# Kernel tuning notes

Measured on AMD Instinct MI355X. Metric: run time of the kernel, lower is better.

The kernel has to match this reference:

```python
import jax, jax.numpy as jnp
import numpy as np

B, N, DIM = 8, 8192, 256
HEADS, LOCAL_HEADS, WINDOW = 8, 1, 64
HD = DIM // HEADS  # 32
MLP_HIDDEN = 1024
EPS = 1e-5


def layer_norm(x, g, b):
    mu = jnp.mean(x, axis=-1, keepdims=True)
    var = jnp.var(x, axis=-1, keepdims=True)
    return (x - mu) * jax.lax.rsqrt(var + EPS) * g + b


def look_around(t, pad_value=0.0):
    # t: (b, nw, w, ...); concat windows [i-1, i, i+1] -> (b, nw, 3w, ...)
    nw = t.shape[1]
    pads = [(0, 0), (1, 1)] + [(0, 0)] * (t.ndim - 2)
    p = jnp.pad(t, pads, constant_values=pad_value)
    return jnp.concatenate([p[:, i:i + nw] for i in range(3)], axis=2)


def local_attn(q, k, v):
    # lucidrains LocalAttention, causal=False, look_backward=look_forward=1
    # q,k,v: (b_merged, n, d)
    b, n, d = q.shape
    nw = n // WINDOW
    scale = d ** -0.5
    bq = q.reshape(b, nw, WINDOW, d) * scale
    bk = look_around(k.reshape(b, nw, WINDOW, d))  # (b, nw, 3w, d)
    bv = look_around(v.reshape(b, nw, WINDOW, d))
    ticker = jnp.arange(n).reshape(1, nw, WINDOW)
    bq_k = look_around(ticker, pad_value=-1)       # (1, nw, 3w)
    pad_mask = (bq_k == -1)[:, :, None, :]         # (1, nw, 1, 3w)
    dots = jnp.einsum('bnie,bnje->bnij', bq, bk)   # (b, nw, w, 3w)
    dots = jnp.where(pad_mask, -1e9, dots)
    attn = jax.nn.softmax(dots, axis=-1)
    out = jnp.einsum('bnij,bnje->bnie', attn, bv)
    return out.reshape(b, n, d)


def linear_attn(q, k, v):
    # q,k,v: (b, h, n, d)
    d = q.shape[-1]
    qs = jax.nn.softmax(q, axis=-1) * d ** -0.5
    ks = jax.nn.softmax(k, axis=-2)
    ctx = jnp.einsum('bhnd,bhne->bhde', ks, v)     # (b, h, d, d) tiny
    return jnp.einsum('bhnd,bhde->bhne', qs, ctx)


def setup_inputs() -> dict:
    key = jax.random.key(0)
    ks = jax.random.split(key, 8)
    s = 0.02
    return {
        'x': jax.random.normal(ks[0], (B, N, DIM), jnp.float32),
        'norm1_g': jnp.ones((DIM,), jnp.float32),
        'norm1_b': jnp.zeros((DIM,), jnp.float32),
        'Wq': jax.random.normal(ks[1], (DIM, DIM), jnp.float32) * s,
        'Wkv': jax.random.normal(ks[2], (DIM, DIM), jnp.float32) * s,
        'Wproj': jax.random.normal(ks[3], (DIM, DIM), jnp.float32) * s,
        'bproj': jnp.zeros((DIM,), jnp.float32),
        'norm2_g': jnp.ones((DIM,), jnp.float32),
        'norm2_b': jnp.zeros((DIM,), jnp.float32),
        'W1': jax.random.normal(ks[4], (MLP_HIDDEN, DIM), jnp.float32) * s,
        'b1': jnp.zeros((MLP_HIDDEN,), jnp.float32),
        'W2': jax.random.normal(ks[5], (DIM, MLP_HIDDEN), jnp.float32) * s,
        'b2': jnp.zeros((DIM,), jnp.float32),
    }


def reference(x, norm1_g, norm1_b, Wq, Wkv, Wproj, bproj, norm2_g, norm2_b, W1, b1, W2, b2):
    b, n, c = x.shape
    h = layer_norm(x, norm1_g, norm1_b)
    q = h @ Wq.T
    kv = h @ Wkv.T  # k and v share the same projection in the original code
    split_heads = lambda t: t.reshape(b, n, HEADS, HD).transpose(0, 2, 1, 3)
    q, k, v = split_heads(q), split_heads(kv), split_heads(kv)
    lq, gq = q[:, :LOCAL_HEADS], q[:, LOCAL_HEADS:]
    lk, gk = k[:, :LOCAL_HEADS], k[:, LOCAL_HEADS:]
    lv, gv = v[:, :LOCAL_HEADS], v[:, LOCAL_HEADS:]
    lout = local_attn(lq.reshape(b * LOCAL_HEADS, n, HD),
                      lk.reshape(b * LOCAL_HEADS, n, HD),
                      lv.reshape(b * LOCAL_HEADS, n, HD)).reshape(b, LOCAL_HEADS, n, HD)
    gout = linear_attn(gq, gk, gv)
    attn = jnp.concatenate([lout, gout], axis=1)   # (b, H, n, hd)
    y = attn.transpose(0, 2, 1, 3).reshape(b, n, c) @ Wproj.T + bproj
    x = x + y
    h2 = layer_norm(x, norm2_g, norm2_b)
    m = jax.nn.gelu(h2 @ W1.T + b1, approximate=False) @ W2.T + b2
    return x + m
```

## Files before the change

kernel.cpp:

```cpp
#include <hip/hip_runtime.h>
#include <hip/hip_bf16.h>

typedef __bf16 bf16;
typedef __bf16 bf16x8 __attribute__((ext_vector_type(8)));
typedef float f32x4 __attribute__((ext_vector_type(4)));

__device__ __forceinline__ void gld16(const void* g, void* l) {
  __builtin_amdgcn_global_load_lds((const __attribute__((address_space(1))) void*)g,
                                   (__attribute__((address_space(3))) void*)l, 16, 0, 0);
}

__global__ void cvt_weights(const float* __restrict__ wq, const float* __restrict__ wkv,
                            const float* __restrict__ wp, const float* __restrict__ w1,
                            const float* __restrict__ w2,
                            bf16* __restrict__ wqkv, bf16* __restrict__ wpb,
                            bf16* __restrict__ w1b, bf16* __restrict__ w2b) {
  int i = blockIdx.x * 256 + threadIdx.x;
  if (i < 65536) wqkv[i] = (bf16)wq[i];
  else if (i < 131072) wqkv[i] = (bf16)wkv[i - 65536];
  else if (i < 196608) wpb[i - 131072] = (bf16)wp[i - 131072];
  else if (i < 458752) w1b[i - 196608] = (bf16)w1[i - 196608];
  else if (i < 720896) w2b[i - 458752] = (bf16)w2[i - 458752];
}

__launch_bounds__(256)
__global__ void ln_kernel(const float* __restrict__ x, const float* __restrict__ g,
                          const float* __restrict__ b, bf16* __restrict__ out) {
  const int row = blockIdx.x * 4 + (threadIdx.x >> 6);
  const int lane = threadIdx.x & 63;
  const float4 v = ((const float4*)(x + (long)row * 256))[lane];
  float s = v.x + v.y + v.z + v.w;
#pragma unroll
  for (int o = 1; o < 64; o <<= 1) s += __shfl_xor(s, o);
  const float mu = s * (1.f / 256.f);
  const float dx = v.x - mu, dy = v.y - mu, dz = v.z - mu, dw = v.w - mu;
  float q = dx * dx + dy * dy + dz * dz + dw * dw;
#pragma unroll
  for (int o = 1; o < 64; o <<= 1) q += __shfl_xor(q, o);
  const float rstd = rsqrtf(q * (1.f / 256.f) + 1e-5f);
  const float4 gg = ((const float4*)g)[lane];
  const float4 bb = ((const float4*)b)[lane];
  union { bf16 h[4]; uint2 u; } pk;
  pk.h[0] = (bf16)(dx * rstd * gg.x + bb.x);
  pk.h[1] = (bf16)(dy * rstd * gg.y + bb.y);
  pk.h[2] = (bf16)(dz * rstd * gg.z + bb.z);
  pk.h[3] = (bf16)(dw * rstd * gg.w + bb.w);
  *(uint2*)(out + (long)row * 256 + lane * 4) = pk.u;
}

template <int EPI>
__launch_bounds__(256)
__global__ void gemm_kernel(const bf16* __restrict__ A, const bf16* __restrict__ B,
                            void* C, const float* __restrict__ bias,
                            const float* res, int Nn, int K) {
  __shared__ bf16 Alds[128 * 64];
  __shared__ bf16 Blds[128 * 64];
  const int tid = threadIdx.x;
  const int w = tid >> 6, lane = tid & 63;
  const int wr = w >> 1, wc = w & 1;
  const long m0 = (long)blockIdx.y * 128;
  const long n0 = (long)blockIdx.x * 128;
  const int srow = lane >> 3;
  const int scol = (lane & 7) * 8;
  f32x4 acc[4][4] = {};
  for (int kt = 0; kt < K; kt += 64) {
#pragma unroll
    for (int i = 0; i < 4; ++i) {
      const int c = w * 4 + i;
      const int row = c * 8 + srow;
      gld16(A + (m0 + row) * K + kt + scol, Alds + c * 512);
      gld16(B + (n0 + row) * K + kt + scol, Blds + c * 512);
    }
    asm volatile("s_waitcnt vmcnt(0)" ::: "memory");
    __syncthreads();
#pragma unroll
    for (int ks = 0; ks < 2; ++ks) {
      const int colo = ks * 32 + (lane >> 4) * 8;
      bf16x8 af[4], bfr[4];
#pragma unroll
      for (int fm = 0; fm < 4; ++fm)
        af[fm] = *(const bf16x8*)(Alds + (wr * 64 + fm * 16 + (lane & 15)) * 64 + colo);
#pragma unroll
      for (int fn = 0; fn < 4; ++fn)
        bfr[fn] = *(const bf16x8*)(Blds + (wc * 64 + fn * 16 + (lane & 15)) * 64 + colo);
#pragma unroll
      for (int fm = 0; fm < 4; ++fm)
#pragma unroll
        for (int fn = 0; fn < 4; ++fn)
          acc[fm][fn] = __builtin_amdgcn_mfma_f32_16x16x32_bf16(af[fm], bfr[fn], acc[fm][fn], 0, 0, 0);
    }
    __syncthreads();
  }
#pragma unroll
  for (int fm = 0; fm < 4; ++fm)
#pragma unroll
    for (int fn = 0; fn < 4; ++fn)
#pragma unroll
      for (int r = 0; r < 4; ++r) {
        const long row = m0 + wr * 64 + fm * 16 + (lane >> 4) * 4 + r;
        const long col = n0 + wc * 64 + fn * 16 + (lane & 15);
        const long idx = row * Nn + col;
        const float v = acc[fm][fn][r];
        if constexpr (EPI == 0) {
          ((bf16*)C)[idx] = (bf16)v;
        } else if constexpr (EPI == 1) {
          ((float*)C)[idx] = v + bias[col] + res[idx];
        } else {
          const float t = v + bias[col];
          ((bf16*)C)[idx] = (bf16)(0.5f * t * (1.f + erff(t * 0.70710678118654752f)));
        }
      }
}

__launch_bounds__(256)
__global__ void lattn_kernel(const bf16* __restrict__ qkv, bf16* __restrict__ attn) {
  const int j = blockIdx.x, b = blockIdx.y;
  const int tid = threadIdx.x, w = tid >> 6, lane = tid & 63;
  __shared__ bf16 Qs[64 * 40];
  __shared__ bf16 Ks[192 * 40];
  __shared__ bf16 Kt[32 * 200];
  __shared__ bf16 Ps[4][16 * 200];
  const float scale = 0.17677669529663687f;
  const long base = (long)b * 8192 + (long)j * 64;
  for (int i = tid; i < 64 * 32; i += 256) {
    const int r = i >> 5, d = i & 31;
    Qs[r * 40 + d] = (bf16)((float)qkv[(base + r) * 512 + d] * scale);
  }
  for (int i = tid; i < 192 * 32; i += 256) {
    const int c = i >> 5, d = i & 31;
    const long tc = (long)j * 64 - 64 + c;
    float kv = 0.f;
    if (tc >= 0 && tc < 8192) kv = (float)qkv[((long)b * 8192 + tc) * 512 + 256 + d];
    const bf16 kb = (bf16)kv;
    Ks[c * 40 + d] = kb;
    Kt[d * 200 + c] = kb;
  }
  __syncthreads();
  const int l15 = lane & 15, l4 = lane >> 4;
  const bf16x8 aq = *(const bf16x8*)(Qs + (w * 16 + l15) * 40 + l4 * 8);
  const f32x4 zz = {0.f, 0.f, 0.f, 0.f};
  f32x4 S[12];
#pragma unroll
  for (int fn = 0; fn < 12; ++fn) {
    const bf16x8 bk = *(const bf16x8*)(Ks + (fn * 16 + l15) * 40 + l4 * 8);
    S[fn] = __builtin_amdgcn_mfma_f32_16x16x32_bf16(aq, bk, zz, 0, 0, 0);
  }
#pragma unroll
  for (int fn = 0; fn < 12; ++fn) {
    const long tc = (long)j * 64 - 64 + fn * 16 + l15;
    if (tc < 0 || tc >= 8192) { S[fn][0] = -1e9f; S[fn][1] = -1e9f; S[fn][2] = -1e9f; S[fn][3] = -1e9f; }
  }
  float sinv[4];
#pragma unroll
  for (int r = 0; r < 4; ++r) {
    float m = -1e30f;
#pragma unroll
    for (int fn = 0; fn < 12; ++fn) m = fmaxf(m, S[fn][r]);
#pragma unroll
    for (int o = 1; o < 16; o <<= 1) m = fmaxf(m, __shfl_xor(m, o));
    float s = 0.f;
#pragma unroll
    for (int fn = 0; fn < 12; ++fn) { const float e = __expf(S[fn][r] - m); S[fn][r] = e; s += e; }
#pragma unroll
    for (int o = 1; o < 16; o <<= 1) s += __shfl_xor(s, o);
    sinv[r] = 1.f / s;
  }
#pragma unroll
  for (int fn = 0; fn < 12; ++fn)
#pragma unroll
    for (int r = 0; r < 4; ++r)
      Ps[w][(l4 * 4 + r) * 200 + fn * 16 + l15] = (bf16)(S[fn][r] * sinv[r]);
  __syncthreads();
  f32x4 O[2] = {};
#pragma unroll
  for (int ks = 0; ks < 6; ++ks) {
    const bf16x8 ap = *(const bf16x8*)(Ps[w] + l15 * 200 + ks * 32 + l4 * 8);
#pragma unroll
    for (int fe = 0; fe < 2; ++fe) {
      const bf16x8 bv = *(const bf16x8*)(Kt + (fe * 16 + l15) * 200 + ks * 32 + l4 * 8);
      O[fe] = __builtin_amdgcn_mfma_f32_16x16x32_bf16(ap, bv, O[fe], 0, 0, 0);
    }
  }
#pragma unroll
  for (int fe = 0; fe < 2; ++fe)
#pragma unroll
    for (int r = 0; r < 4; ++r)
      attn[(base + w * 16 + l4 * 4 + r) * 256 + fe * 16 + l15] = (bf16)O[fe][r];
}

__launch_bounds__(256)
__global__ void ctx_kernel(const bf16* __restrict__ qkv, float* __restrict__ ctx,
                           float* __restrict__ S) {
  const int bh = blockIdx.x;
  const int b = bh / 7, h = bh % 7 + 1;
  const int tid = threadIdx.x;
  const int w = tid >> 6, lane = tid & 63;
  const int l15 = lane & 15, l4 = lane >> 4;
  __shared__ bf16 evT[32 * 264];
  __shared__ bf16 kT[48 * 264];
  __shared__ float red[4][32 * 48];
  const long n0 = (long)blockIdx.y * 256;
  const bf16* kp = qkv + ((long)b * 8192 + n0 + tid) * 512 + 256 + h * 32;
  bf16x8 kv[4];
#pragma unroll
  for (int c = 0; c < 4; ++c) kv[c] = *(const bf16x8*)(kp + c * 8);
#pragma unroll
  for (int i = 0; i < 16; ++i)
    kT[(32 + i) * 264 + tid] = (i == 0) ? (bf16)1.0f : (bf16)0.0f;
#pragma unroll
  for (int c = 0; c < 4; ++c)
#pragma unroll
    for (int j = 0; j < 8; ++j) {
      const int d = c * 8 + j;
      evT[d * 264 + tid] = (bf16)__expf((float)kv[c][j]);
      kT[d * 264 + tid] = kv[c][j];
    }
  __syncthreads();
  f32x4 acc[2][3] = {};
#pragma unroll
  for (int ks = 0; ks < 2; ++ks) {
    const int ncol = w * 64 + ks * 32 + l4 * 8;
    bf16x8 af[2], bb[3];
#pragma unroll
    for (int fm = 0; fm < 2; ++fm) af[fm] = *(const bf16x8*)(evT + (fm * 16 + l15) * 264 + ncol);
#pragma unroll
    for (int fe = 0; fe < 3; ++fe) bb[fe] = *(const bf16x8*)(kT + (fe * 16 + l15) * 264 + ncol);
#pragma unroll
    for (int fm = 0; fm < 2; ++fm)
#pragma unroll
      for (int fe = 0; fe < 3; ++fe)
        acc[fm][fe] = __builtin_amdgcn_mfma_f32_16x16x32_bf16(af[fm], bb[fe], acc[fm][fe], 0, 0, 0);
  }
#pragma unroll
  for (int fm = 0; fm < 2; ++fm)
#pragma unroll
    for (int fe = 0; fe < 3; ++fe)
#pragma unroll
      for (int r = 0; r < 4; ++r)
        red[w][(fm * 16 + l4 * 4 + r) * 48 + fe * 16 + l15] = acc[fm][fe][r];
  __syncthreads();
  for (int i = tid; i < 32 * 48; i += 256) {
    const float v = red[0][i] + red[1][i] + red[2][i] + red[3][i];
    const int d = i / 48, e = i - d * 48;
    if (e < 32) atomicAdd(ctx + (long)bh * 1024 + d * 32 + e, v);
    else if (e == 32) atomicAdd(S + bh * 32 + d, v);
  }
}

__launch_bounds__(256)
__global__ void lout_kernel(const bf16* __restrict__ qkv, const float* __restrict__ S,
                            const float* __restrict__ ctx, bf16* __restrict__ attn) {
  const int bh = blockIdx.x;
  const int b = bh / 7, h = bh % 7 + 1;
  const int tid = threadIdx.x;
  const int w = tid >> 6, lane = tid & 63;
  const int l15 = lane & 15, l4 = lane >> 4;
  __shared__ bf16 qs[256 * 40];
  __shared__ bf16 C2t[32 * 40];
  const long n0 = (long)blockIdx.y * 256;
  for (int i = tid; i < 1024; i += 256) {
    const int e = i >> 5, d = i & 31;
    C2t[e * 40 + d] = (bf16)(ctx[(long)bh * 1024 + d * 32 + e] / S[bh * 32 + d]);
  }
  const bf16* qp = qkv + ((long)b * 8192 + n0 + tid) * 512 + h * 32;
  bf16x8 qv[4];
#pragma unroll
  for (int c = 0; c < 4; ++c) qv[c] = *(const bf16x8*)(qp + c * 8);
  float qf[32];
#pragma unroll
  for (int c = 0; c < 4; ++c)
#pragma unroll
    for (int j = 0; j < 8; ++j) qf[c * 8 + j] = (float)qv[c][j];
  float m = qf[0];
#pragma unroll
  for (int d = 1; d < 32; ++d) m = fmaxf(m, qf[d]);
  float s = 0.f;
#pragma unroll
  for (int d = 0; d < 32; ++d) { qf[d] = __expf(qf[d] - m); s += qf[d]; }
  const float f = 0.17677669529663687f / s;
#pragma unroll
  for (int c = 0; c < 4; ++c) {
    bf16x8 o;
#pragma unroll
    for (int j = 0; j < 8; ++j) o[j] = (bf16)(qf[c * 8 + j] * f);
    *(bf16x8*)(qs + tid * 40 + c * 8) = o;
  }
  __syncthreads();
  f32x4 acc[4][2] = {};
  bf16x8 bfr[2];
#pragma unroll
  for (int fe = 0; fe < 2; ++fe) bfr[fe] = *(const bf16x8*)(C2t + (fe * 16 + l15) * 40 + l4 * 8);
#pragma unroll
  for (int fm = 0; fm < 4; ++fm) {
    const bf16x8 af = *(const bf16x8*)(qs + (w * 64 + fm * 16 + l15) * 40 + l4 * 8);
#pragma unroll
    for (int fe = 0; fe < 2; ++fe)
      acc[fm][fe] = __builtin_amdgcn_mfma_f32_16x16x32_bf16(af, bfr[fe], acc[fm][fe], 0, 0, 0);
  }
#pragma unroll
  for (int fm = 0; fm < 4; ++fm)
#pragma unroll
    for (int fe = 0; fe < 2; ++fe)
#pragma unroll
      for (int r = 0; r < 4; ++r)
        attn[((long)b * 8192 + n0 + w * 64 + fm * 16 + l4 * 4 + r) * 256 + h * 32 + fe * 16 + l15]
            = (bf16)acc[fm][fe][r];
}

extern "C" void kernel_launch(void* const* d_in, const int* in_sizes, int n_in,
                              void* d_out, int out_size, void* d_ws, size_t ws_size,
                              hipStream_t stream) {
  const float* x     = (const float*)d_in[0];
  const float* n1g   = (const float*)d_in[1];
  const float* n1b   = (const float*)d_in[2];
  const float* Wq    = (const float*)d_in[3];
  const float* Wkv   = (const float*)d_in[4];
  const float* Wproj = (const float*)d_in[5];
  const float* bproj = (const float*)d_in[6];
  const float* n2g   = (const float*)d_in[7];
  const float* n2b   = (const float*)d_in[8];
  const float* W1    = (const float*)d_in[9];
  const float* b1    = (const float*)d_in[10];
  const float* W2    = (const float*)d_in[11];
  const float* b2    = (const float*)d_in[12];
  float* out = (float*)d_out;
  char* ws = (char*)d_ws;

  bf16* wqkv   = (bf16*)(ws + 0);
  bf16* wprojb = (bf16*)(ws + 262144);
  bf16* w1b    = (bf16*)(ws + 393216);
  bf16* w2b    = (bf16*)(ws + 917504);
  float* Sbuf  = (float*)(ws + 1441792);
  float* ctx   = (float*)(ws + 1448960);
  bf16* hbuf   = (bf16*)(ws + 1685504);
  bf16* qkv    = (bf16*)(ws + 35239936);
  bf16* hidden = qkv;

  cvt_weights<<<2816, 256, 0, stream>>>(Wq, Wkv, Wproj, W1, W2, wqkv, wprojb, w1b, w2b);
  ln_kernel<<<16384, 256, 0, stream>>>(x, n1g, n1b, hbuf);
  gemm_kernel<0><<<dim3(4, 512), 256, 0, stream>>>(hbuf, wqkv, qkv, nullptr, nullptr, 512, 256);
  hipMemsetAsync(Sbuf, 0, 7168 + 229376, stream);
  lattn_kernel<<<dim3(128, 8), 256, 0, stream>>>(qkv, hbuf);
  ctx_kernel<<<dim3(56, 32), 256, 0, stream>>>(qkv, ctx, Sbuf);
  lout_kernel<<<dim3(56, 32), 256, 0, stream>>>(qkv, Sbuf, ctx, hbuf);
  gemm_kernel<1><<<dim3(2, 512), 256, 0, stream>>>(hbuf, wprojb, out, bproj, x, 256, 256);
  ln_kernel<<<16384, 256, 0, stream>>>(out, n2g, n2b, hbuf);
  gemm_kernel<2><<<dim3(8, 512), 256, 0, stream>>>(hbuf, w1b, hidden, b1, nullptr, 1024, 256);
  gemm_kernel<1><<<dim3(2, 512), 256, 0, stream>>>(hidden, w2b, out, b2, out, 256, 1024);
}
```

Before: 412.2 us.

## Restructure GEMMs: stream A through swizzled double-buffered LDS, read B directly from global

Replaces the 128x128 LDS-tiled GEMM with a 512-thread kernel whose block covers 64 rows and the full N tile (up to 512 columns). Only A goes through LDS, as XOR-swizzled, double-buffered K chunks loaded asynchronously. B fragments are loaded straight from global memory and rely on cache reuse across blocks. The aim is to avoid re-reading A per column tile, cut LDS traffic and bank conflicts, and overlap loads with MFMA work, at the cost of more register pressure and uncached-path global loads for B.

```diff
diff --git a/kernel.cpp b/kernel.cpp
--- a/kernel.cpp
+++ b/kernel.cpp
@@ -48,58 +48,79 @@
   *(uint2*)(out + (long)row * 256 + lane * 4) = pk.u;
 }
 
-template <int EPI>
-__launch_bounds__(256)
-__global__ void gemm_kernel(const bf16* __restrict__ A, const bf16* __restrict__ B,
-                            void* C, const float* __restrict__ bias,
-                            const float* res, int Nn, int K) {
-  __shared__ bf16 Alds[128 * 64];
-  __shared__ bf16 Blds[128 * 64];
+template <int EPI, int MT, int NTILE, int KK, int NCHUNK>
+__launch_bounds__(512, 4)
+__global__ void gemm_bd(const bf16* __restrict__ A, const bf16* __restrict__ B,
+                        void* C, const float* __restrict__ bias,
+                        const float* res, int ldC) {
+  constexpr int CW = NTILE / 8;
+  constexpr int FM = MT / 16;
+  constexpr int FN = CW / 16;
+  constexpr int CK = KK / NCHUNK;
+  constexpr int RSB = 2 * CK;
+  constexpr int LROW = (RSB == 256) ? 8 : ((RSB == 512) ? 9 : 10);
+  constexpr int CHB = MT * CK * 2;
+  constexpr int ITER = CHB / (512 * 16);
+  __shared__ bf16 lds[2 * MT * CK];
   const int tid = threadIdx.x;
   const int w = tid >> 6, lane = tid & 63;
-  const int wr = w >> 1, wc = w & 1;
-  const long m0 = (long)blockIdx.y * 128;
-  const long n0 = (long)blockIdx.x * 128;
-  const int srow = lane >> 3;
-  const int scol = (lane & 7) * 8;
-  f32x4 acc[4][4] = {};
-  for (int kt = 0; kt < K; kt += 64) {
-#pragma unroll
-    for (int i = 0; i < 4; ++i) {
-      const int c = w * 4 + i;
-      const int row = c * 8 + srow;
-      gld16(A + (m0 + row) * K + kt + scol, Alds + c * 512);
-      gld16(B + (n0 + row) * K + kt + scol, Blds + c * 512);
-    }
-    asm volatile("s_waitcnt vmcnt(0)" ::: "memory");
-    __syncthreads();
-#pragma unroll
-    for (int ks = 0; ks < 2; ++ks) {
-      const int colo = ks * 32 + (lane >> 4) * 8;
-      bf16x8 af[4], bfr[4];
-#pragma unroll
-      for (int fm = 0; fm < 4; ++fm)
-        af[fm] = *(const bf16x8*)(Alds + (wr * 64 + fm * 16 + (lane & 15)) * 64 + colo);
-#pragma unroll
-      for (int fn = 0; fn < 4; ++fn)
-        bfr[fn] = *(const bf16x8*)(Blds + (wc * 64 + fn * 16 + (lane & 15)) * 64 + colo);
-#pragma unroll
-      for (int fm = 0; fm < 4; ++fm)
-#pragma unroll
-        for (int fn = 0; fn < 4; ++fn)
-          acc[fm][fn] = __builtin_amdgcn_mfma_f32_16x16x32_bf16(af[fm], bfr[fn], acc[fm][fn], 0, 0, 0);
-    }
-    __syncthreads();
-  }
-#pragma unroll
-  for (int fm = 0; fm < 4; ++fm)
-#pragma unroll
-    for (int fn = 0; fn < 4; ++fn)
+  const int l15 = lane & 15, l4 = lane >> 4;
+  const int swz = (l15 & 7) << 4;
+  const long m0 = (long)blockIdx.x * MT;
+  const int n_base = blockIdx.y * NTILE;
+  const bf16* Bl = B + ((long)(n_base + w * CW + l15)) * KK + l4 * 8;
+
+  f32x4 acc[FM][FN] = {};
+
+  auto stage = [&](int c, int buf) {
+#pragma unroll
+    for (int it = 0; it < ITER; ++it) {
+      const int p = it * 8192 + tid * 16;
+      const int row = p >> LROW;
+      const int colb = (p & (RSB - 1)) ^ ((row & 7) << 4);
+      gld16((const char*)A + ((m0 + row) * KK + (long)c * CK) * 2 + colb,
+            (char*)lds + buf * CHB + it * 8192 + w * 1024);
+    }
+  };
+
+  stage(0, 0);
+  asm volatile("s_waitcnt vmcnt(0)" ::: "memory");
+  __syncthreads();
+
+  for (int c = 0; c < NCHUNK; ++c) {
+    if (c + 1 < NCHUNK) stage(c + 1, (c + 1) & 1);
+    const char* base = (const char*)lds + (c & 1) * CHB;
+#pragma unroll
+    for (int kl = 0; kl < CK / 32; ++kl) {
+      bf16x8 bfrag[FN];
+#pragma unroll
+      for (int fn = 0; fn < FN; ++fn)
+        bfrag[fn] = *(const bf16x8*)(Bl + (long)fn * 16 * KK + c * CK + kl * 32);
+      bf16x8 afrag[FM];
+#pragma unroll
+      for (int fm = 0; fm < FM; ++fm)
+        afrag[fm] = *(const bf16x8*)(base + (fm * 16 + l15) * RSB + ((kl * 64 + l4 * 16) ^ swz));
+#pragma unroll
+      for (int fm = 0; fm < FM; ++fm)
+#pragma unroll
+        for (int fn = 0; fn < FN; ++fn)
+          acc[fm][fn] = __builtin_amdgcn_mfma_f32_16x16x32_bf16(afrag[fm], bfrag[fn], acc[fm][fn], 0, 0, 0);
+    }
+    if (c + 1 < NCHUNK) {
+      asm volatile("s_waitcnt vmcnt(0)" ::: "memory");
+      __syncthreads();
+    }
+  }
+
+#pragma unroll
+  for (int fm = 0; fm < FM; ++fm)
+#pragma unroll
+    for (int fn = 0; fn < FN; ++fn)
 #pragma unroll
       for (int r = 0; r < 4; ++r) {
-        const long row = m0 + wr * 64 + fm * 16 + (lane >> 4) * 4 + r;
-        const long col = n0 + wc * 64 + fn * 16 + (lane & 15);
-        const long idx = row * Nn + col;
+        const long row = m0 + fm * 16 + l4 * 4 + r;
+        const int col = n_base + w * CW + fn * 16 + l15;
+        const long idx = row * ldC + col;
         const float v = acc[fm][fn][r];
         if constexpr (EPI == 0) {
           ((bf16*)C)[idx] = (bf16)v;
@@ -338,13 +359,13 @@
 
   cvt_weights<<<2816, 256, 0, stream>>>(Wq, Wkv, Wproj, W1, W2, wqkv, wprojb, w1b, w2b);
   ln_kernel<<<16384, 256, 0, stream>>>(x, n1g, n1b, hbuf);
-  gemm_kernel<0><<<dim3(4, 512), 256, 0, stream>>>(hbuf, wqkv, qkv, nullptr, nullptr, 512, 256);
+  gemm_bd<0, 64, 512, 256, 2><<<dim3(1024, 1), 512, 0, stream>>>(hbuf, wqkv, qkv, nullptr, nullptr, 512);
   hipMemsetAsync(Sbuf, 0, 7168 + 229376, stream);
   lattn_kernel<<<dim3(128, 8), 256, 0, stream>>>(qkv, hbuf);
   ctx_kernel<<<dim3(56, 32), 256, 0, stream>>>(qkv, ctx, Sbuf);
   lout_kernel<<<dim3(56, 32), 256, 0, stream>>>(qkv, Sbuf, ctx, hbuf);
-  gemm_kernel<1><<<dim3(2, 512), 256, 0, stream>>>(hbuf, wprojb, out, bproj, x, 256, 256);
+  gemm_bd<1, 64, 256, 256, 2><<<dim3(1024, 1), 512, 0, stream>>>(hbuf, wprojb, out, bproj, x, 256);
   ln_kernel<<<16384, 256, 0, stream>>>(out, n2g, n2b, hbuf);
-  gemm_kernel<2><<<dim3(8, 512), 256, 0, stream>>>(hbuf, w1b, hidden, b1, nullptr, 1024, 256);
-  gemm_kernel<1><<<dim3(2, 512), 256, 0, stream>>>(hidden, w2b, out, b2, out, 256, 1024);
-}
+  gemm_bd<2, 64, 512, 256, 2><<<dim3(1024, 2), 512, 0, stream>>>(hbuf, w1b, hidden, b1, nullptr, 1024);
+  gemm_bd<1, 64, 256, 1024, 4><<<dim3(1024, 1), 512, 0, stream>>>(hidden, w2b, out, b2, out, 256);
+}
```

New measurement: 403.2 us. -2.2%, faster.

## Replace LDS-tiled GEMM with register-resident weight GEMMs and XCD-aware block mapping

Applied to the files above, without the earlier changes.

Replaces the shared-memory tiled 128x128 GEMM with kernels where each wave holds a 64-column slice of the weight matrix in registers for the full K=256 and streams 64 rows of A directly from global memory into registers. LDS staging and the barriers around it go away, and a block-index remap spreads consecutive slots across the 8 XCDs. The K=1024 MLP down-projection gets its own kernel that reloads weight chunks per K-chunk and accumulates into the output in place. The trade-offs are heavy register pressure (the 2-blocks-per-SM launch bound may force spills), redundant global reads of weights by every wave, and uncoalesced 16-byte-per-lane A loads that no longer share tiles across waves.

```diff
diff --git a/kernel.cpp b/kernel.cpp
--- a/kernel.cpp
+++ b/kernel.cpp
@@ -4,11 +4,6 @@
 typedef __bf16 bf16;
 typedef __bf16 bf16x8 __attribute__((ext_vector_type(8)));
 typedef float f32x4 __attribute__((ext_vector_type(4)));
-
-__device__ __forceinline__ void gld16(const void* g, void* l) {
-  __builtin_amdgcn_global_load_lds((const __attribute__((address_space(1))) void*)g,
-                                   (__attribute__((address_space(3))) void*)l, 16, 0, 0);
-}
 
 __global__ void cvt_weights(const float* __restrict__ wq, const float* __restrict__ wkv,
                             const float* __restrict__ wp, const float* __restrict__ w1,
@@ -48,68 +43,129 @@
   *(uint2*)(out + (long)row * 256 + lane * 4) = pk.u;
 }
 
-template <int EPI>
-__launch_bounds__(256)
-__global__ void gemm_kernel(const bf16* __restrict__ A, const bf16* __restrict__ B,
-                            void* C, const float* __restrict__ bias,
-                            const float* res, int Nn, int K) {
-  __shared__ bf16 Alds[128 * 64];
-  __shared__ bf16 Blds[128 * 64];
-  const int tid = threadIdx.x;
-  const int w = tid >> 6, lane = tid & 63;
-  const int wr = w >> 1, wc = w & 1;
-  const long m0 = (long)blockIdx.y * 128;
-  const long n0 = (long)blockIdx.x * 128;
-  const int srow = lane >> 3;
-  const int scol = (lane & 7) * 8;
-  f32x4 acc[4][4] = {};
-  for (int kt = 0; kt < K; kt += 64) {
-#pragma unroll
-    for (int i = 0; i < 4; ++i) {
-      const int c = w * 4 + i;
-      const int row = c * 8 + srow;
-      gld16(A + (m0 + row) * K + kt + scol, Alds + c * 512);
-      gld16(B + (n0 + row) * K + kt + scol, Blds + c * 512);
+template <int EPI, int NCG, int NBLK>
+__launch_bounds__(256, 2)
+__global__ void gemm_reg(const bf16* __restrict__ A, const bf16* __restrict__ Bw,
+                         void* C, const float* __restrict__ bias,
+                         const float* __restrict__ res, int ldC) {
+  const int tid = threadIdx.x, w = tid >> 6, lane = tid & 63;
+  const int l15 = lane & 15, l4 = lane >> 4;
+  const int bid = blockIdx.x;
+  const int slot4 = ((bid & 7) * (NBLK / 8) + (bid >> 3)) * 4 + w;
+  const int cg = slot4 % NCG;
+  const long row0 = (long)(slot4 / NCG) * 64;
+  const int c0 = cg * 64;
+
+  bf16x8 Breg[8][4];
+  {
+    const bf16* Bp = Bw + ((long)c0 + l15) * 256 + l4 * 8;
+#pragma unroll
+    for (int kl = 0; kl < 8; ++kl)
+#pragma unroll
+      for (int fn = 0; fn < 4; ++fn)
+        Breg[kl][fn] = *(const bf16x8*)(Bp + fn * (16 * 256) + kl * 32);
+  }
+  float biasr[4];
+  if constexpr (EPI != 0) {
+#pragma unroll
+    for (int fn = 0; fn < 4; ++fn) biasr[fn] = bias[c0 + fn * 16 + l15];
+  }
+
+#pragma unroll
+  for (int mi = 0; mi < 2; ++mi) {
+    const long r0 = row0 + mi * 32;
+    bf16x8 Areg[2][8];
+    const bf16* Ap = A + (r0 + l15) * 256 + l4 * 8;
+#pragma unroll
+    for (int fm = 0; fm < 2; ++fm)
+#pragma unroll
+      for (int kl = 0; kl < 8; ++kl)
+        Areg[fm][kl] = *(const bf16x8*)(Ap + fm * (16 * 256) + kl * 32);
+    f32x4 acc[2][4] = {};
+#pragma unroll
+    for (int kl = 0; kl < 8; ++kl)
+#pragma unroll
+      for (int fm = 0; fm < 2; ++fm)
+#pragma unroll
+        for (int fn = 0; fn < 4; ++fn)
+          acc[fm][fn] = __builtin_amdgcn_mfma_f32_16x16x32_bf16(Areg[fm][kl], Breg[kl][fn],
+                                                                acc[fm][fn], 0, 0, 0);
+#pragma unroll
+    for (int fm = 0; fm < 2; ++fm)
+#pragma unroll
+      for (int fn = 0; fn < 4; ++fn)
+#pragma unroll
+        for (int r = 0; r < 4; ++r) {
+          const long row = r0 + fm * 16 + l4 * 4 + r;
+          const long col = c0 + fn * 16 + l15;
+          const long idx = row * ldC + col;
+          const float v = acc[fm][fn][r];
+          if constexpr (EPI == 0) {
+            ((bf16*)C)[idx] = (bf16)v;
+          } else if constexpr (EPI == 1) {
+            ((float*)C)[idx] = v + biasr[fn] + res[idx];
+          } else {
+            const float t = v + biasr[fn];
+            ((bf16*)C)[idx] = (bf16)(0.5f * t * (1.f + erff(t * 0.70710678118654752f)));
+          }
+        }
+  }
+}
+
+__launch_bounds__(256, 2)
+__global__ void gemm_mlp2(const bf16* __restrict__ A, const bf16* __restrict__ Bw,
+                          float* __restrict__ C, const float* __restrict__ bias) {
+  constexpr int NBLK = 1024, NCG = 4;
+  const int tid = threadIdx.x, w = tid >> 6, lane = tid & 63;
+  const int l15 = lane & 15, l4 = lane >> 4;
+  const int bid = blockIdx.x;
+  const int slot4 = ((bid & 7) * (NBLK / 8) + (bid >> 3)) * 4 + w;
+  const int cg = slot4 % NCG;
+  const long row0 = (long)(slot4 / NCG) * 64;
+  const int c0 = cg * 64;
+  float biasr[4];
+#pragma unroll
+  for (int fn = 0; fn < 4; ++fn) biasr[fn] = bias[c0 + fn * 16 + l15];
+
+#pragma unroll
+  for (int mi = 0; mi < 2; ++mi) {
+    const long r0 = row0 + mi * 32;
+    f32x4 acc[2][4] = {};
+    for (int kc = 0; kc < 4; ++kc) {
+      bf16x8 Breg[8][4];
+      const bf16* Bp = Bw + ((long)c0 + l15) * 1024 + kc * 256 + l4 * 8;
+#pragma unroll
+      for (int kl = 0; kl < 8; ++kl)
+#pragma unroll
+        for (int fn = 0; fn < 4; ++fn)
+          Breg[kl][fn] = *(const bf16x8*)(Bp + fn * (16 * 1024) + kl * 32);
+      bf16x8 Areg[2][8];
+      const bf16* Ap = A + (r0 + l15) * 1024 + kc * 256 + l4 * 8;
+#pragma unroll
+      for (int fm = 0; fm < 2; ++fm)
+#pragma unroll
+        for (int kl = 0; kl < 8; ++kl)
+          Areg[fm][kl] = *(const bf16x8*)(Ap + fm * (16 * 1024) + kl * 32);
+#pragma unroll
+      for (int kl = 0; kl < 8; ++kl)
+#pragma unroll
+        for (int fm = 0; fm < 2; ++fm)
+#pragma unroll
+          for (int fn = 0; fn < 4; ++fn)
+            acc[fm][fn] = __builtin_amdgcn_mfma_f32_16x16x32_bf16(Areg[fm][kl], Breg[kl][fn],
+                                                                  acc[fm][fn], 0, 0, 0);
     }
-    asm volatile("s_waitcnt vmcnt(0)" ::: "memory");
-    __syncthreads();
-#pragma unroll
-    for (int ks = 0; ks < 2; ++ks) {
-      const int colo = ks * 32 + (lane >> 4) * 8;
-      bf16x8 af[4], bfr[4];
-#pragma unroll
-      for (int fm = 0; fm < 4; ++fm)
-        af[fm] = *(const bf16x8*)(Alds + (wr * 64 + fm * 16 + (lane & 15)) * 64 + colo);
+#pragma unroll
+    for (int fm = 0; fm < 2; ++fm)
 #pragma unroll
       for (int fn = 0; fn < 4; ++fn)
-        bfr[fn] = *(const bf16x8*)(Blds + (wc * 64 + fn * 16 + (lane & 15)) * 64 + colo);
-#pragma unroll
-      for (int fm = 0; fm < 4; ++fm)
-#pragma unroll
-        for (int fn = 0; fn < 4; ++fn)
-          acc[fm][fn] = __builtin_amdgcn_mfma_f32_16x16x32_bf16(af[fm], bfr[fn], acc[fm][fn], 0, 0, 0);
-    }
-    __syncthreads();
-  }
-#pragma unroll
-  for (int fm = 0; fm < 4; ++fm)
-#pragma unroll
-    for (int fn = 0; fn < 4; ++fn)
-#pragma unroll
-      for (int r = 0; r < 4; ++r) {
-        const long row = m0 + wr * 64 + fm * 16 + (lane >> 4) * 4 + r;
-        const long col = n0 + wc * 64 + fn * 16 + (lane & 15);
-        const long idx = row * Nn + col;
-        const float v = acc[fm][fn][r];
-        if constexpr (EPI == 0) {
-          ((bf16*)C)[idx] = (bf16)v;
-        } else if constexpr (EPI == 1) {
-          ((float*)C)[idx] = v + bias[col] + res[idx];
-        } else {
-          const float t = v + bias[col];
-          ((bf16*)C)[idx] = (bf16)(0.5f * t * (1.f + erff(t * 0.70710678118654752f)));
+#pragma unroll
+        for (int r = 0; r < 4; ++r) {
+          const long row = r0 + fm * 16 + l4 * 4 + r;
+          const long idx = row * 256 + c0 + fn * 16 + l15;
+          C[idx] = C[idx] + acc[fm][fn][r] + biasr[fn];
         }
-      }
+  }
 }
 
 __launch_bounds__(256)
@@ -338,13 +394,13 @@
 
   cvt_weights<<<2816, 256, 0, stream>>>(Wq, Wkv, Wproj, W1, W2, wqkv, wprojb, w1b, w2b);
   ln_kernel<<<16384, 256, 0, stream>>>(x, n1g, n1b, hbuf);
-  gemm_kernel<0><<<dim3(4, 512), 256, 0, stream>>>(hbuf, wqkv, qkv, nullptr, nullptr, 512, 256);
+  gemm_reg<0, 8, 2048><<<2048, 256, 0, stream>>>(hbuf, wqkv, qkv, nullptr, nullptr, 512);
   hipMemsetAsync(Sbuf, 0, 7168 + 229376, stream);
   lattn_kernel<<<dim3(128, 8), 256, 0, stream>>>(qkv, hbuf);
   ctx_kernel<<<dim3(56, 32), 256, 0, stream>>>(qkv, ctx, Sbuf);
   lout_kernel<<<dim3(56, 32), 256, 0, stream>>>(qkv, Sbuf, ctx, hbuf);
-  gemm_kernel<1><<<dim3(2, 512), 256, 0, stream>>>(hbuf, wprojb, out, bproj, x, 256, 256);
+  gemm_reg<1, 4, 1024><<<1024, 256, 0, stream>>>(hbuf, wprojb, out, bproj, x, 256);
   ln_kernel<<<16384, 256, 0, stream>>>(out, n2g, n2b, hbuf);
-  gemm_kernel<2><<<dim3(8, 512), 256, 0, stream>>>(hbuf, w1b, hidden, b1, nullptr, 1024, 256);
-  gemm_kernel<1><<<dim3(2, 512), 256, 0, stream>>>(hidden, w2b, out, b2, out, 256, 1024);
-}
+  gemm_reg<2, 16, 4096><<<4096, 256, 0, stream>>>(hbuf, w1b, hidden, b1, nullptr, 1024);
+  gemm_mlp2<<<1024, 256, 0, stream>>>(hidden, w2b, out, b2);
+}
```

Result: slower. 598.4 us (+45.2%).
